# Kernel tuning notes

Measured on AMD Instinct MI355X. Metric: run time of the kernel, lower is better.

Reference implementation:

```python
import jax, jax.numpy as jnp
import numpy as np

N_NODES = 100000


def gcn_layer(x, W, b, src, dst, n):
    # PyG GCNConv: h = x @ W, then D^{-1/2}(A+I)D^{-1/2} aggregation, then + b
    h = x @ W  # [N, out]
    ones = jnp.ones(src.shape[0], dtype=h.dtype)
    deg = jax.ops.segment_sum(ones, dst, num_segments=n) + 1.0  # +1 for self loop
    dinv = jax.lax.rsqrt(deg)  # [N]
    norm = dinv[src] * dinv[dst]  # [E]
    msgs = h[src] * norm[:, None]  # gather + scale, [E, out]
    agg = jax.ops.segment_sum(msgs, dst, num_segments=n)
    agg = agg + h * (dinv * dinv)[:, None]  # self-loop term
    return agg + b


def setup_inputs() -> dict:
    key = jax.random.key(0)
    k1, k2, k3, k4, k5, k6 = jax.random.split(key, 6)
    in_dim, h1, h2 = 256, 128, 64
    x = jax.random.normal(k1, (N_NODES, in_dim), dtype=jnp.float32)
    edge_index = jax.random.randint(k2, (2, 1600000), 0, N_NODES, dtype=jnp.int64)
    # Glorot-style init for weights, zeros for bias (PyG default)
    W1 = jax.random.normal(k3, (in_dim, h1), dtype=jnp.float32) / np.sqrt(in_dim)
    b1 = jnp.zeros((h1,), dtype=jnp.float32)
    W2 = jax.random.normal(k4, (h1, h2), dtype=jnp.float32) / np.sqrt(h1)
    b2 = jnp.zeros((h2,), dtype=jnp.float32)
    return {"x": x, "W1": W1, "b1": b1, "W2": W2, "b2": b2, "edge_index": edge_index}


def reference(x, W1, b1, W2, b2, edge_index):
    src, dst = edge_index[0], edge_index[1]
    n = x.shape[0]
    h = jax.nn.relu(gcn_layer(x, W1, b1, src, dst, n))
    h = jax.nn.relu(gcn_layer(h, W2, b2, src, dst, n))
    return h
```

## Files before the change

kernel.cpp:

```cpp
#include <hip/hip_runtime.h>
#include <hip/hip_bf16.h>


__device__ inline float bflo(unsigned u) { return __uint_as_float(u << 16); }
__device__ inline float bfhi(unsigned u) { return __uint_as_float(u & 0xffff0000u); }
__device__ inline unsigned pack_bf16_2(float lo, float hi) {
    unsigned a = __float_as_uint(lo), b = __float_as_uint(hi);
    a = (a + 0x7fff + ((a >> 16) & 1)) >> 16;
    b = (b + 0x7fff + ((b >> 16) & 1)) >> 16;
    return a | (b << 16);
}

__global__ void hist_kernel(const int* __restrict__ dst, int* __restrict__ deg, int E) {
    int stride = gridDim.x * blockDim.x;
    for (int i = blockIdx.x * blockDim.x + threadIdx.x; i < E; i += stride)
        atomicAdd(&deg[dst[i]], 1);
}

__global__ __launch_bounds__(1024) void scan_partial_kernel(const int* __restrict__ deg,
        int* __restrict__ psum, float* __restrict__ dinv, int n) {
    __shared__ int wsum[16];
    int tid = threadIdx.x, wave = tid >> 6, lane = tid & 63;
    int i0 = blockIdx.x * 4096 + tid * 4;
    int v0 = 0, v1 = 0, v2 = 0, v3 = 0;
    if (i0 + 3 < n) {
        int4 v = *(const int4*)(deg + i0);
        v0 = v.x; v1 = v.y; v2 = v.z; v3 = v.w;
    } else {
        if (i0 + 0 < n) v0 = deg[i0 + 0];
        if (i0 + 1 < n) v1 = deg[i0 + 1];
        if (i0 + 2 < n) v2 = deg[i0 + 2];
        if (i0 + 3 < n) v3 = deg[i0 + 3];
    }
    if (i0 + 0 < n) dinv[i0 + 0] = 1.0f / sqrtf((float)v0 + 1.0f);
    if (i0 + 1 < n) dinv[i0 + 1] = 1.0f / sqrtf((float)v1 + 1.0f);
    if (i0 + 2 < n) dinv[i0 + 2] = 1.0f / sqrtf((float)v2 + 1.0f);
    if (i0 + 3 < n) dinv[i0 + 3] = 1.0f / sqrtf((float)v3 + 1.0f);
    int s = v0 + v1 + v2 + v3;
    #pragma unroll
    for (int off = 1; off < 64; off <<= 1) s += __shfl_xor(s, off, 64);
    if (lane == 0) wsum[wave] = s;
    __syncthreads();
    if (tid == 0) {
        int t = 0;
        #pragma unroll
        for (int w = 0; w < 16; ++w) t += wsum[w];
        psum[blockIdx.x] = t;
    }
}

__global__ void scan_base_kernel(int* __restrict__ psum, int* __restrict__ offs,
                                 int nb, int n) {
    int lane = threadIdx.x;
    int v = (lane < nb) ? psum[lane] : 0;
    int x = v;
    #pragma unroll
    for (int off = 1; off < 64; off <<= 1) {
        int y = __shfl_up(x, off, 64);
        if (lane >= off) x += y;
    }
    if (lane < nb) psum[lane] = x - v;
    if (lane == 63) offs[n] = x;
}

__global__ __launch_bounds__(1024) void scan_local_kernel(const int* __restrict__ deg,
        const int* __restrict__ psum, int* __restrict__ offs, int n) {
    __shared__ int wsum[16];
    int tid = threadIdx.x, wave = tid >> 6, lane = tid & 63;
    int i0 = blockIdx.x * 4096 + tid * 4;
    int v0 = 0, v1 = 0, v2 = 0, v3 = 0;
    if (i0 + 3 < n) {
        int4 v = *(const int4*)(deg + i0);
        v0 = v.x; v1 = v.y; v2 = v.z; v3 = v.w;
    } else {
        if (i0 + 0 < n) v0 = deg[i0 + 0];
        if (i0 + 1 < n) v1 = deg[i0 + 1];
        if (i0 + 2 < n) v2 = deg[i0 + 2];
        if (i0 + 3 < n) v3 = deg[i0 + 3];
    }
    int s = v0 + v1 + v2 + v3;
    int x = s;
    #pragma unroll
    for (int off = 1; off < 64; off <<= 1) {
        int y = __shfl_up(x, off, 64);
        if (lane >= off) x += y;
    }
    if (lane == 63) wsum[wave] = x;
    __syncthreads();
    int wbase = 0;
    #pragma unroll
    for (int w = 0; w < 16; ++w)
        if (w < wave) wbase += wsum[w];
    int ex = psum[blockIdx.x] + wbase + (x - s);
    if (i0 + 0 < n) offs[i0 + 0] = ex;
    if (i0 + 1 < n) offs[i0 + 1] = ex + v0;
    if (i0 + 2 < n) offs[i0 + 2] = ex + v0 + v1;
    if (i0 + 3 < n) offs[i0 + 3] = ex + v0 + v1 + v2;
}

__global__ void fill_kernel(const int* __restrict__ src, const int* __restrict__ dst,
        const int* __restrict__ offs, int* __restrict__ cursor,
        int* __restrict__ csr, int E) {
    int stride = gridDim.x * blockDim.x;
    for (int i = blockIdx.x * blockDim.x + threadIdx.x; i < E; i += stride) {
        int d = dst[i];
        int pos = offs[d] + atomicAdd(&cursor[d], 1);
        csr[pos] = src[i];
    }
}

template <int K, int N, int RPT>
__global__ __launch_bounds__(256) void gemm_scale_kernel(const float* __restrict__ X,
        const float* __restrict__ W, const float* __restrict__ dinv,
        unsigned* __restrict__ Gp, int M) {
    constexpr int CPT = 8;
    constexpr int CG  = N / CPT;
    constexpr int RG  = 256 / CG;
    constexpr int BM  = RG * RPT;
    constexpr int BK  = 16;
    static_assert(BM == 64, "tile geometry");
    __shared__ float xs[BK][BM];
    __shared__ float ws[BK][N];

    int tid = threadIdx.x;
    int cg = tid % CG, rg = tid / CG;
    int c0 = cg * CPT, r0 = rg * RPT;
    int brow = blockIdx.x * BM;

    float acc[RPT][CPT] = {};

    for (int k0 = 0; k0 < K; k0 += BK) {
        {
            int r = tid >> 2;
            int q = tid & 3;
            int row = brow + r;
            if (row >= M) row = M - 1;
            const float4 xv = *(const float4*)(X + (size_t)row * K + k0 + q * 4);
            xs[q * 4 + 0][r] = xv.x;
            xs[q * 4 + 1][r] = xv.y;
            xs[q * 4 + 2][r] = xv.z;
            xs[q * 4 + 3][r] = xv.w;
        }
        {
            constexpr int NF4  = N / 4;
            constexpr int TOT4 = BK * NF4;
            #pragma unroll
            for (int t = 0; t < TOT4 / 256; ++t) {
                int idx = tid + t * 256;
                int kk = idx / NF4, n4 = idx % NF4;
                *(float4*)&ws[kk][n4 * 4] =
                    *(const float4*)(W + (size_t)(k0 + kk) * N + n4 * 4);
            }
        }
        __syncthreads();
        #pragma unroll
        for (int k = 0; k < BK; ++k) {
            float a[RPT], b[CPT];
            #pragma unroll
            for (int r = 0; r < RPT; ++r) a[r] = xs[k][r0 + r];
            #pragma unroll
            for (int c = 0; c < CPT; ++c) b[c] = ws[k][c0 + c];
            #pragma unroll
            for (int r = 0; r < RPT; ++r)
                #pragma unroll
                for (int c = 0; c < CPT; ++c)
                    acc[r][c] = fmaf(a[r], b[c], acc[r][c]);
        }
        __syncthreads();
    }

    #pragma unroll
    for (int r = 0; r < RPT; ++r) {
        int row = brow + r0 + r;
        if (row < M) {
            float s = dinv[row];
            uint4 p;
            p.x = pack_bf16_2(acc[r][0] * s, acc[r][1] * s);
            p.y = pack_bf16_2(acc[r][2] * s, acc[r][3] * s);
            p.z = pack_bf16_2(acc[r][4] * s, acc[r][5] * s);
            p.w = pack_bf16_2(acc[r][6] * s, acc[r][7] * s);
            *(uint4*)(Gp + (size_t)row * (N / 2) + c0 / 2) = p;
        }
    }
}

__global__ __launch_bounds__(256) void aggregate128_kernel(const unsigned* __restrict__ G,
        const int* __restrict__ csr, const int* __restrict__ offs,
        const float* __restrict__ dinv, const float* __restrict__ bias,
        float* __restrict__ out, int n) {
    int wave = threadIdx.x >> 6, lane = threadIdx.x & 63;
    int node = blockIdx.x * 4 + wave;
    if (node >= n) return;
    int beg = offs[node], end = offs[node + 1];

    unsigned u = G[(size_t)node * 64 + lane];
    float a0 = bflo(u), a1 = bfhi(u);
    int e = beg;
    for (; e + 4 <= end; e += 4) {
        int s0 = csr[e], s1 = csr[e + 1], s2 = csr[e + 2], s3 = csr[e + 3];
        unsigned u0 = G[(size_t)s0 * 64 + lane];
        unsigned u1 = G[(size_t)s1 * 64 + lane];
        unsigned u2 = G[(size_t)s2 * 64 + lane];
        unsigned u3 = G[(size_t)s3 * 64 + lane];
        a0 += (bflo(u0) + bflo(u1)) + (bflo(u2) + bflo(u3));
        a1 += (bfhi(u0) + bfhi(u1)) + (bfhi(u2) + bfhi(u3));
    }
    for (; e < end; ++e) {
        unsigned u0 = G[(size_t)csr[e] * 64 + lane];
        a0 += bflo(u0);
        a1 += bfhi(u0);
    }
    float di = dinv[node];
    float2 r;
    r.x = fmaxf(fmaf(a0, di, bias[lane * 2 + 0]), 0.0f);
    r.y = fmaxf(fmaf(a1, di, bias[lane * 2 + 1]), 0.0f);
    ((float2*)(out + (size_t)node * 128))[lane] = r;
}

__global__ __launch_bounds__(256) void aggregate64_kernel(const unsigned* __restrict__ G,
        const int* __restrict__ csr, const int* __restrict__ offs,
        const float* __restrict__ dinv, const float* __restrict__ bias,
        float* __restrict__ out, int n) {
    int wave = threadIdx.x >> 6, lane = threadIdx.x & 63;
    int node = blockIdx.x * 4 + wave;
    if (node >= n) return;
    int beg = offs[node], end = offs[node + 1];
    int half = lane >> 5, col = lane & 31;

    float a0 = 0.0f, a1 = 0.0f;
    if (half == 0) {
        unsigned u = G[(size_t)node * 32 + col];
        a0 = bflo(u); a1 = bfhi(u);
    }
    int e = beg;
    for (; e + 4 <= end; e += 4) {
        int sA = csr[e + half], sB = csr[e + 2 + half];
        unsigned uA = G[(size_t)sA * 32 + col];
        unsigned uB = G[(size_t)sB * 32 + col];
        a0 += bflo(uA) + bflo(uB);
        a1 += bfhi(uA) + bfhi(uB);
    }
    if (e + 2 <= end) {
        int sA = csr[e + half];
        unsigned uA = G[(size_t)sA * 32 + col];
        a0 += bflo(uA);
        a1 += bfhi(uA);
        e += 2;
    }
    if (e < end && half == 0) {
        unsigned uA = G[(size_t)csr[e] * 32 + col];
        a0 += bflo(uA);
        a1 += bfhi(uA);
    }
    a0 += __shfl_down(a0, 32, 64);
    a1 += __shfl_down(a1, 32, 64);
    if (half == 0) {
        float di = dinv[node];
        float2 r;
        r.x = fmaxf(fmaf(a0, di, bias[col * 2 + 0]), 0.0f);
        r.y = fmaxf(fmaf(a1, di, bias[col * 2 + 1]), 0.0f);
        ((float2*)(out + (size_t)node * 64))[col] = r;
    }
}

extern "C" void kernel_launch(void* const* d_in, const int* in_sizes, int n_in,
                              void* d_out, int out_size, void* d_ws, size_t ws_size,
                              hipStream_t stream) {
    const float* x  = (const float*)d_in[0];
    const float* W1 = (const float*)d_in[1];
    const float* b1 = (const float*)d_in[2];
    const float* W2 = (const float*)d_in[3];
    const float* b2 = (const float*)d_in[4];
    const int* edge = (const int*)d_in[5];

    const int IN = 256, H1 = 128;
    const int E = in_sizes[5] / 2;
    const int N = in_sizes[0] / IN;
    const int* srcp = edge;
    const int* dstp = edge + E;

    char* ws = (char*)d_ws;
    auto alignup = [](size_t v) { return (v + 255) & ~(size_t)255; };
    size_t off = 0;
    size_t degSz = alignup((size_t)N * 4);
    int*      deg    = (int*)(ws + off);      off += degSz;
    int*      cursor = (int*)(ws + off);      off += degSz;
    int*      offs   = (int*)(ws + off);      off += alignup(((size_t)N + 1) * 4);
    float*    dinv   = (float*)(ws + off);    off += degSz;
    int*      psum   = (int*)(ws + off);      off += alignup(64 * 4);
    int*      csr    = (int*)(ws + off);      off += alignup((size_t)E * 4);
    unsigned* g1     = (unsigned*)(ws + off); off += alignup((size_t)N * (H1 / 2) * 4);
    float*    h1     = (float*)(ws + off);    off += alignup((size_t)N * H1 * 4);
    unsigned* g2     = g1;

    hipMemsetAsync(deg, 0, 2 * degSz, stream);

    int egrid = (E + 255) / 256;
    if (egrid > 2048) egrid = 2048;
    int sb = (N + 4095) / 4096;

    hist_kernel<<<egrid, 256, 0, stream>>>(dstp, deg, E);
    scan_partial_kernel<<<sb, 1024, 0, stream>>>(deg, psum, dinv, N);
    scan_base_kernel<<<1, 64, 0, stream>>>(psum, offs, sb, N);
    scan_local_kernel<<<sb, 1024, 0, stream>>>(deg, psum, offs, N);
    fill_kernel<<<egrid, 256, 0, stream>>>(srcp, dstp, offs, cursor, csr, E);

    int mgrid = (N + 63) / 64;
    int agrid = (N + 3) / 4;

    gemm_scale_kernel<256, 128, 4><<<mgrid, 256, 0, stream>>>(x, W1, dinv, g1, N);
    aggregate128_kernel<<<agrid, 256, 0, stream>>>(g1, csr, offs, dinv, b1, h1, N);
    gemm_scale_kernel<128, 64, 2><<<mgrid, 256, 0, stream>>>(h1, W2, dinv, g2, N);
    aggregate64_kernel<<<agrid, 256, 0, stream>>>(g2, csr, offs, dinv, b2,
                                                  (float*)d_out, N);
}
```

Before: 556.0 us.

## Replace FP32 SIMT GEMMs with split-bf16 MFMA GEMMs

Replaces the scalar FP32 register-tiled GEMM with a matrix-core kernel using bf16 MFMA 16x16x32. Both operands are split into hi and lo bf16 parts, and three MFMAs per tile recover near-FP32 accuracy. A small pre-pass kernel transposes and splits the weights. The aim is to move the dense matmuls onto matrix cores. The cost is extra conversion work, weights read straight from global memory without LDS staging, and scalar 2-byte output stores.

```diff
diff --git a/kernel.cpp b/kernel.cpp
--- a/kernel.cpp
+++ b/kernel.cpp
@@ -2,14 +2,19 @@
 #include <hip/hip_bf16.h>
 
 
+typedef __attribute__((ext_vector_type(8))) short bf16x8;
+typedef __attribute__((ext_vector_type(4))) float f32x4;
+
+__device__ inline unsigned short f2bf(float f) {
+    unsigned u = __float_as_uint(f);
+    u = (u + 0x7fff + ((u >> 16) & 1)) >> 16;
+    return (unsigned short)u;
+}
+__device__ inline float bf2f(unsigned short h) {
+    return __uint_as_float(((unsigned)h) << 16);
+}
 __device__ inline float bflo(unsigned u) { return __uint_as_float(u << 16); }
 __device__ inline float bfhi(unsigned u) { return __uint_as_float(u & 0xffff0000u); }
-__device__ inline unsigned pack_bf16_2(float lo, float hi) {
-    unsigned a = __float_as_uint(lo), b = __float_as_uint(hi);
-    a = (a + 0x7fff + ((a >> 16) & 1)) >> 16;
-    b = (b + 0x7fff + ((b >> 16) & 1)) >> 16;
-    return a | (b << 16);
-}
 
 __global__ void hist_kernel(const int* __restrict__ dst, int* __restrict__ deg, int E) {
     int stride = gridDim.x * blockDim.x;
@@ -109,77 +114,105 @@
     }
 }
 
-template <int K, int N, int RPT>
-__global__ __launch_bounds__(256) void gemm_scale_kernel(const float* __restrict__ X,
-        const float* __restrict__ W, const float* __restrict__ dinv,
-        unsigned* __restrict__ Gp, int M) {
-    constexpr int CPT = 8;
-    constexpr int CG  = N / CPT;
-    constexpr int RG  = 256 / CG;
-    constexpr int BM  = RG * RPT;
-    constexpr int BK  = 16;
-    static_assert(BM == 64, "tile geometry");
-    __shared__ float xs[BK][BM];
-    __shared__ float ws[BK][N];
-
-    int tid = threadIdx.x;
-    int cg = tid % CG, rg = tid / CG;
-    int c0 = cg * CPT, r0 = rg * RPT;
-    int brow = blockIdx.x * BM;
-
-    float acc[RPT][CPT] = {};
+__global__ void wsplit_kernel(const float* __restrict__ W,
+        unsigned short* __restrict__ Wt_hi, unsigned short* __restrict__ Wt_lo,
+        int K, int N) {
+    int idx = blockIdx.x * 256 + threadIdx.x;
+    if (idx >= K * N) return;
+    int k = idx / N, n = idx - k * N;
+    float v = W[idx];
+    unsigned short h = f2bf(v);
+    unsigned short l = f2bf(v - bf2f(h));
+    Wt_hi[(size_t)n * K + k] = h;
+    Wt_lo[(size_t)n * K + k] = l;
+}
+
+template <int K, int NT>
+__global__ __launch_bounds__(256) void gemm_mfma_kernel(const float* __restrict__ X,
+        const unsigned short* __restrict__ Wt_hi, const unsigned short* __restrict__ Wt_lo,
+        const float* __restrict__ dinv, unsigned short* __restrict__ G, int M) {
+    constexpr int N   = NT * 16;
+    constexpr int BK  = 32;
+    constexpr int LDA = BK + 8;
+    __shared__ unsigned short Ah[128 * LDA];
+    __shared__ unsigned short Al[128 * LDA];
+
+    const int tid  = threadIdx.x;
+    const int wv   = tid >> 6, ln = tid & 63;
+    const int l16  = ln & 15, kseg = ln >> 4;
+    const int brow = blockIdx.x * 128;
+
+    f32x4 acc[2][NT];
+    #pragma unroll
+    for (int a = 0; a < 2; ++a)
+        #pragma unroll
+        for (int b = 0; b < NT; ++b) acc[a][b] = 0;
+
+    const int srow = tid >> 1;
+    const int scol = (tid & 1) * 16;
+    int grow = brow + srow;
+    if (grow >= M) grow = M - 1;
+    const float* xrow = X + (size_t)grow * K + scol;
+    unsigned int* ahw = (unsigned int*)&Ah[srow * LDA + scol];
+    unsigned int* alw = (unsigned int*)&Al[srow * LDA + scol];
+
+    const int arow = wv * 32;
 
     for (int k0 = 0; k0 < K; k0 += BK) {
-        {
-            int r = tid >> 2;
-            int q = tid & 3;
-            int row = brow + r;
-            if (row >= M) row = M - 1;
-            const float4 xv = *(const float4*)(X + (size_t)row * K + k0 + q * 4);
-            xs[q * 4 + 0][r] = xv.x;
-            xs[q * 4 + 1][r] = xv.y;
-            xs[q * 4 + 2][r] = xv.z;
-            xs[q * 4 + 3][r] = xv.w;
+        float4 q0 = *(const float4*)(xrow + k0 + 0);
+        float4 q1 = *(const float4*)(xrow + k0 + 4);
+        float4 q2 = *(const float4*)(xrow + k0 + 8);
+        float4 q3 = *(const float4*)(xrow + k0 + 12);
+        float v[16] = {q0.x,q0.y,q0.z,q0.w, q1.x,q1.y,q1.z,q1.w,
+                       q2.x,q2.y,q2.z,q2.w, q3.x,q3.y,q3.z,q3.w};
+        unsigned hw[8], lw[8];
+        #pragma unroll
+        for (int j = 0; j < 8; ++j) {
+            unsigned short h0 = f2bf(v[2*j]),   h1 = f2bf(v[2*j+1]);
+            unsigned short l0 = f2bf(v[2*j]   - bf2f(h0));
+            unsigned short l1 = f2bf(v[2*j+1] - bf2f(h1));
+            hw[j] = (unsigned)h0 | ((unsigned)h1 << 16);
+            lw[j] = (unsigned)l0 | ((unsigned)l1 << 16);
         }
-        {
-            constexpr int NF4  = N / 4;
-            constexpr int TOT4 = BK * NF4;
+        *(uint4*)(ahw + 0) = make_uint4(hw[0], hw[1], hw[2], hw[3]);
+        *(uint4*)(ahw + 4) = make_uint4(hw[4], hw[5], hw[6], hw[7]);
+        *(uint4*)(alw + 0) = make_uint4(lw[0], lw[1], lw[2], lw[3]);
+        *(uint4*)(alw + 4) = make_uint4(lw[4], lw[5], lw[6], lw[7]);
+        __syncthreads();
+
+        bf16x8 a_h[2], a_l[2];
+        #pragma unroll
+        for (int tr = 0; tr < 2; ++tr) {
+            a_h[tr] = *(const bf16x8*)&Ah[(arow + tr * 16 + l16) * LDA + kseg * 8];
+            a_l[tr] = *(const bf16x8*)&Al[(arow + tr * 16 + l16) * LDA + kseg * 8];
+        }
+        #pragma unroll
+        for (int tc = 0; tc < NT; ++tc) {
+            size_t wo = (size_t)(tc * 16 + l16) * K + k0 + kseg * 8;
+            bf16x8 b_h = *(const bf16x8*)(Wt_hi + wo);
+            bf16x8 b_l = *(const bf16x8*)(Wt_lo + wo);
             #pragma unroll
-            for (int t = 0; t < TOT4 / 256; ++t) {
-                int idx = tid + t * 256;
-                int kk = idx / NF4, n4 = idx % NF4;
-                *(float4*)&ws[kk][n4 * 4] =
-                    *(const float4*)(W + (size_t)(k0 + kk) * N + n4 * 4);
+            for (int tr = 0; tr < 2; ++tr) {
+                acc[tr][tc] = __builtin_amdgcn_mfma_f32_16x16x32_bf16(a_h[tr], b_h, acc[tr][tc], 0, 0, 0);
+                acc[tr][tc] = __builtin_amdgcn_mfma_f32_16x16x32_bf16(a_l[tr], b_h, acc[tr][tc], 0, 0, 0);
+                acc[tr][tc] = __builtin_amdgcn_mfma_f32_16x16x32_bf16(a_h[tr], b_l, acc[tr][tc], 0, 0, 0);
             }
         }
         __syncthreads();
-        #pragma unroll
-        for (int k = 0; k < BK; ++k) {
-            float a[RPT], b[CPT];
-            #pragma unroll
-            for (int r = 0; r < RPT; ++r) a[r] = xs[k][r0 + r];
-            #pragma unroll
-            for (int c = 0; c < CPT; ++c) b[c] = ws[k][c0 + c];
-            #pragma unroll
-            for (int r = 0; r < RPT; ++r)
+    }
+
+    #pragma unroll
+    for (int tr = 0; tr < 2; ++tr) {
+        int rbase = brow + arow + tr * 16 + (ln >> 4) * 4;
+        #pragma unroll
+        for (int r = 0; r < 4; ++r) {
+            int row = rbase + r;
+            if (row < M) {
+                float dv = dinv[row];
                 #pragma unroll
-                for (int c = 0; c < CPT; ++c)
-                    acc[r][c] = fmaf(a[r], b[c], acc[r][c]);
-        }
-        __syncthreads();
-    }
-
-    #pragma unroll
-    for (int r = 0; r < RPT; ++r) {
-        int row = brow + r0 + r;
-        if (row < M) {
-            float s = dinv[row];
-            uint4 p;
-            p.x = pack_bf16_2(acc[r][0] * s, acc[r][1] * s);
-            p.y = pack_bf16_2(acc[r][2] * s, acc[r][3] * s);
-            p.z = pack_bf16_2(acc[r][4] * s, acc[r][5] * s);
-            p.w = pack_bf16_2(acc[r][6] * s, acc[r][7] * s);
-            *(uint4*)(Gp + (size_t)row * (N / 2) + c0 / 2) = p;
+                for (int tc = 0; tc < NT; ++tc)
+                    G[(size_t)row * N + tc * 16 + l16] = f2bf(acc[tr][tc][r] * dv);
+            }
         }
     }
 }
@@ -273,7 +306,7 @@
     const float* b2 = (const float*)d_in[4];
     const int* edge = (const int*)d_in[5];
 
-    const int IN = 256, H1 = 128;
+    const int IN = 256, H1 = 128, H2 = 64;
     const int E = in_sizes[5] / 2;
     const int N = in_sizes[0] / IN;
     const int* srcp = edge;
@@ -283,15 +316,19 @@
     auto alignup = [](size_t v) { return (v + 255) & ~(size_t)255; };
     size_t off = 0;
     size_t degSz = alignup((size_t)N * 4);
-    int*      deg    = (int*)(ws + off);      off += degSz;
-    int*      cursor = (int*)(ws + off);      off += degSz;
-    int*      offs   = (int*)(ws + off);      off += alignup(((size_t)N + 1) * 4);
-    float*    dinv   = (float*)(ws + off);    off += degSz;
-    int*      psum   = (int*)(ws + off);      off += alignup(64 * 4);
-    int*      csr    = (int*)(ws + off);      off += alignup((size_t)E * 4);
-    unsigned* g1     = (unsigned*)(ws + off); off += alignup((size_t)N * (H1 / 2) * 4);
-    float*    h1     = (float*)(ws + off);    off += alignup((size_t)N * H1 * 4);
-    unsigned* g2     = g1;
+    int*            deg    = (int*)(ws + off);            off += degSz;
+    int*            cursor = (int*)(ws + off);            off += degSz;
+    int*            offs   = (int*)(ws + off);            off += alignup(((size_t)N + 1) * 4);
+    float*          dinv   = (float*)(ws + off);          off += degSz;
+    int*            psum   = (int*)(ws + off);            off += alignup(64 * 4);
+    int*            csr    = (int*)(ws + off);            off += alignup((size_t)E * 4);
+    unsigned short* wt1h   = (unsigned short*)(ws + off); off += alignup((size_t)IN * H1 * 2);
+    unsigned short* wt1l   = (unsigned short*)(ws + off); off += alignup((size_t)IN * H1 * 2);
+    unsigned short* wt2h   = (unsigned short*)(ws + off); off += alignup((size_t)H1 * H2 * 2);
+    unsigned short* wt2l   = (unsigned short*)(ws + off); off += alignup((size_t)H1 * H2 * 2);
+    unsigned short* g1     = (unsigned short*)(ws + off); off += alignup((size_t)N * H1 * 2);
+    float*          h1     = (float*)(ws + off);          off += alignup((size_t)N * H1 * 4);
+    unsigned short* g2     = g1;
 
     hipMemsetAsync(deg, 0, 2 * degSz, stream);
 
@@ -304,13 +341,16 @@
     scan_base_kernel<<<1, 64, 0, stream>>>(psum, offs, sb, N);
     scan_local_kernel<<<sb, 1024, 0, stream>>>(deg, psum, offs, N);
     fill_kernel<<<egrid, 256, 0, stream>>>(srcp, dstp, offs, cursor, csr, E);
-
-    int mgrid = (N + 63) / 64;
+    wsplit_kernel<<<(IN * H1 + 255) / 256, 256, 0, stream>>>(W1, wt1h, wt1l, IN, H1);
+    wsplit_kernel<<<(H1 * H2 + 255) / 256, 256, 0, stream>>>(W2, wt2h, wt2l, H1, H2);
+
+    int mgrid = (N + 127) / 128;
     int agrid = (N + 3) / 4;
 
-    gemm_scale_kernel<256, 128, 4><<<mgrid, 256, 0, stream>>>(x, W1, dinv, g1, N);
-    aggregate128_kernel<<<agrid, 256, 0, stream>>>(g1, csr, offs, dinv, b1, h1, N);
-    gemm_scale_kernel<128, 64, 2><<<mgrid, 256, 0, stream>>>(h1, W2, dinv, g2, N);
-    aggregate64_kernel<<<agrid, 256, 0, stream>>>(g2, csr, offs, dinv, b2,
-                                                  (float*)d_out, N);
-}
+    gemm_mfma_kernel<256, 8><<<mgrid, 256, 0, stream>>>(x, wt1h, wt1l, dinv, g1, N);
+    aggregate128_kernel<<<agrid, 256, 0, stream>>>((const unsigned*)g1, csr, offs,
+                                                   dinv, b1, h1, N);
+    gemm_mfma_kernel<128, 4><<<mgrid, 256, 0, stream>>>(h1, wt2h, wt2l, dinv, g2, N);
+    aggregate64_kernel<<<agrid, 256, 0, stream>>>((const unsigned*)g2, csr, offs,
+                                                  dinv, b2, (float*)d_out, N);
+}
```

Result: no change. 558.9 us (+0.5%).
